# Kernel tuning notes

Hardware: AMD Instinct MI355X
Metric: run time of the kernel (lower is better)

Reference implementation:

```python
import jax, jax.numpy as jnp
import numpy as np

GAMMA = 0.5
LENS = 0.5
WINDOW = 10  # window_size from init

@jax.custom_vjp
def act_fun(x):
    # Heaviside forward, Gaussian surrogate backward (matches torch ActFun)
    return (x > 0).astype(x.dtype)

def _act_fwd(x):
    return act_fun(x), x

def _act_bwd(x, g):
    temp = jnp.exp(-x * x / (2 * LENS * LENS)) / (np.sqrt(2 * np.pi) * LENS)
    return (GAMMA * g * temp,)

act_fun.defvjp(_act_fwd, _act_bwd)

def mem_update(inputs, mem, thr):
    # decay_neu == 1
    mem = mem + inputs
    spike = act_fun(mem - thr)
    mem = mem * (1 - spike)
    neg = (mem < -thr).astype(mem.dtype)
    mem = mem * (1 - neg) - thr * neg
    return mem, spike

def setup_inputs() -> dict:
    key = jax.random.key(0)
    ks = jax.random.split(key, 6)
    B, T, D, H, O = 128, 100, 2048, 1024, 20
    return {
        "input": jax.random.normal(ks[0], (B, T, D), jnp.float32),
        "labels": jax.random.randint(ks[1], (B,), 0, O),
        "hidden_mem": jnp.zeros((B, H), jnp.float32),
        "hidden_spike": jnp.zeros((B, H), jnp.float32),
        "output_mem": jnp.zeros((B, O), jnp.float32),
        "output_spike": jnp.zeros((B, O), jnp.float32),
        "Wi2h": jax.random.normal(ks[2], (H, D), jnp.float32) / np.sqrt(D).astype(np.float32),
        "bi2h": jnp.zeros((H,), jnp.float32),
        "Wh2h": jax.random.normal(ks[3], (H, H), jnp.float32) / np.sqrt(H).astype(np.float32),
        "bh2h": jnp.zeros((H,), jnp.float32),
        "Wh2o": jax.random.normal(ks[4], (O, H), jnp.float32) / np.sqrt(H).astype(np.float32),
        "bh2o": jnp.zeros((O,), jnp.float32),
        "thr_h": jnp.ones((H,), jnp.float32),
        "thr_o": jnp.ones((O,), jnp.float32),
    }

def reference(input, labels, hidden_mem, hidden_spike, output_mem, output_spike,
              Wi2h, bi2h, Wh2h, bh2h, Wh2o, bh2o, thr_h, thr_o):
    B = input.shape[0]

    def step(carry, x_t):
        hm, hs, om, osp, osum = carry
        h_in = x_t @ Wi2h.T + bi2h + hs @ Wh2h.T + bh2h
        hm, hs = mem_update(h_in, hm, thr_h)
        om, osp = mem_update(hs @ Wh2o.T + bh2o, om, thr_o)
        osum = osum + osp
        nbr = (jnp.sum(osp) + jnp.sum(hs)) / B
        return (hm, hs, om, osp, osum), (hs, nbr)

    osum0 = jnp.zeros_like(output_spike)
    carry0 = (hidden_mem, hidden_spike, output_mem, output_spike, osum0)
    (hm, hs, om, osp, osum), (hs_t, nbr_events) = jax.lax.scan(
        step, carry0, jnp.swapaxes(input, 0, 1))  # scan over T

    hidden_spike_t = jnp.transpose(hs_t, (1, 2, 0))  # [B, H, T]
    # moving average over time windows (unfold + mean), stride 1
    c = jnp.cumsum(jnp.pad(hidden_spike_t, ((0, 0), (0, 0), (1, 0))), axis=2)
    hidden_spike_filt = (c[:, :, WINDOW:] - c[:, :, :-WINDOW]) / WINDOW  # [B,H,T-W+1]

    logp = jax.nn.log_softmax(osum, axis=1)
    predictions = jnp.argmax(logp, axis=1)[None, :]  # [1, B]
    loss = -jnp.mean(logp[jnp.arange(B), labels])  # NLLLoss on log_softmax
    return predictions, loss, nbr_events, hidden_spike_filt
```

## Files before the change

kernel.cpp:

```cpp
#include <hip/hip_runtime.h>
#include <hip/hip_bf16.h>
#include <cstdint>
#include <cstddef>

#define B_ 128
#define T_ 100
#define D_ 2048
#define H_ 1024
#define O_ 20
#define H2 512

#define P2NB 256
#define GEMM_NB 800
#define XI_READY 8

typedef float vfloat4 __attribute__((ext_vector_type(4)));

__device__ inline void f4acc(float4& a, const float4 v) {
    a.x += v.x; a.y += v.y; a.z += v.z; a.w += v.w;
}

__global__ __launch_bounds__(256) void prep_kernel(const float* __restrict__ Wh2o,
                                                   float* __restrict__ W2oT,
                                                   float* __restrict__ nbr,
                                                   int* __restrict__ g_flag,
                                                   int* __restrict__ xi_done)
{
    int i = blockIdx.x * 256 + threadIdx.x;
    if (i < H_ * O_) {
        int hh = i / O_;
        int oo = i - hh * O_;
        W2oT[i] = Wh2o[oo * H_ + hh];
    }
    if (i < T_) { nbr[i] = 0.0f; xi_done[i] = 0; }
    if (i < B_ * 2) g_flag[i] = 0;
}

__global__ __launch_bounds__(256) void transpose_kernel(const float* __restrict__ A,
                                                        float* __restrict__ AT)
{
    __shared__ float tile[32][33];
    int bx = blockIdx.x * 32, by = blockIdx.y * 32;
    int tx = threadIdx.x, ty = threadIdx.y;
#pragma unroll
    for (int i = 0; i < 32; i += 8)
        tile[ty + i][tx] = A[(size_t)(by + ty + i) * H_ + bx + tx];
    __syncthreads();
#pragma unroll
    for (int i = 0; i < 32; i += 8)
        AT[(size_t)(bx + ty + i) * H_ + by + tx] = tile[tx][ty + i];
}

__device__ __forceinline__ void gemm_role(int g,
    const float* __restrict__ X, const float* __restrict__ W,
    const float* __restrict__ bi2h, const float* __restrict__ bh2h,
    float* __restrict__ Xi, int* __restrict__ xi_done)
{
    __shared__ float As[16][132];
    __shared__ float Bs[16][132];
    const int t   = g >> 3;
    const int n0  = (g & 7) << 7;
    const int tid = threadIdx.x;
    const int tm8 = (tid >> 5) << 3;
    const int tn4 = (tid & 31) << 2;
    const int ldr = tid >> 2;
    const int ldc = (tid & 3) << 2;

    const float* Xp = X + (size_t)ldr * (T_ * D_) + (size_t)t * D_ + ldc;
    const float* Wp = W + (size_t)(n0 + ldr) * D_ + ldc;

    float acc[8][4];
#pragma unroll
    for (int i = 0; i < 8; ++i)
#pragma unroll
        for (int j = 0; j < 4; ++j) acc[i][j] = 0.0f;

    float4 va = *(const float4*)(Xp);
    float4 vb = *(const float4*)(Wp);
    for (int k0 = 0; k0 < D_; k0 += 16) {
        __syncthreads();
        As[ldc + 0][ldr] = va.x; As[ldc + 1][ldr] = va.y;
        As[ldc + 2][ldr] = va.z; As[ldc + 3][ldr] = va.w;
        Bs[ldc + 0][ldr] = vb.x; Bs[ldc + 1][ldr] = vb.y;
        Bs[ldc + 2][ldr] = vb.z; Bs[ldc + 3][ldr] = vb.w;
        __syncthreads();
        if (k0 + 16 < D_) {
            va = *(const float4*)(Xp + k0 + 16);
            vb = *(const float4*)(Wp + k0 + 16);
        }
#pragma unroll
        for (int k = 0; k < 16; ++k) {
            float4 A0 = *(const float4*)&As[k][tm8];
            float4 A1 = *(const float4*)&As[k][tm8 + 4];
            float4 B0 = *(const float4*)&Bs[k][tn4];
            float a[8] = {A0.x, A0.y, A0.z, A0.w, A1.x, A1.y, A1.z, A1.w};
            float b4[4] = {B0.x, B0.y, B0.z, B0.w};
#pragma unroll
            for (int i = 0; i < 8; ++i)
#pragma unroll
                for (int j = 0; j < 4; ++j) acc[i][j] += a[i] * b4[j];
        }
    }

    float bs[4];
#pragma unroll
    for (int j = 0; j < 4; ++j) {
        int n = n0 + tn4 + j;
        bs[j] = bi2h[n] + bh2h[n];
    }
#pragma unroll
    for (int i = 0; i < 8; ++i) {
        size_t row = (size_t)(tm8 + i) * T_ + t;
        vfloat4 o = {acc[i][0] + bs[0], acc[i][1] + bs[1],
                     acc[i][2] + bs[2], acc[i][3] + bs[3]};
        __builtin_nontemporal_store(o, (vfloat4*)(Xi + row * H_ + n0 + tn4));
    }
    __syncthreads();
    if (tid == 0)
        __hip_atomic_fetch_add(&xi_done[t], 1, __ATOMIC_RELEASE,
                               __HIP_MEMORY_SCOPE_AGENT);
}

__global__ __launch_bounds__(512, 4) void mega_kernel(
    const float* __restrict__ X,
    const float* __restrict__ Wi2h,
    const float* __restrict__ bi2h,
    const float* __restrict__ bh2h,
    float* __restrict__ Xi,
    int* __restrict__ xi_done,
    const float* __restrict__ WT,
    const float* __restrict__ W2oT,
    const float* __restrict__ bh2o,
    const float* __restrict__ thr_h_g,
    const float* __restrict__ thr_o_g,
    const float* __restrict__ hm0,
    const float* __restrict__ hs0,
    const float* __restrict__ om0,
    unsigned long long* __restrict__ g_mask,
    int* __restrict__ g_flag,
    ulonglong2* __restrict__ spk,
    float* __restrict__ osum_out,
    float* __restrict__ nbr_acc)
{
    if (blockIdx.x >= P2NB) {
        gemm_role(blockIdx.x - P2NB, X, Wi2h, bi2h, bh2h, Xi, xi_done);
        return;
    }

    const int pair = blockIdx.x >> 1;
    const int half = blockIdx.x & 1;
    const int b = pair;
    const int tid = threadIdx.x;
    const int lane = tid & 63;
    const int wv = tid >> 6;
    const int h0 = half * H2;
    const int ph0 = h0 ^ H2;
    const int h = h0 + tid;

    __shared__ int   s_list[1024];
    __shared__ float4 s_red[4][128];
    __shared__ unsigned long long s_mask[16];
    __shared__ float s_opart[8][O_];
    __shared__ float s_om[O_], s_osum[O_], s_tho[O_], s_bo[O_];

    float hm = hm0[(size_t)b * H_ + h];
    const float thr = thr_h_g[h];

    if (half == 0 && tid < O_) {
        s_om[tid]   = om0[b * O_ + tid];
        s_osum[tid] = 0.0f;
        s_tho[tid]  = thr_o_g[tid];
        s_bo[tid]   = bh2o[tid];
    }

    {
        bool own = hs0[(size_t)b * H_ + h] > 0.5f;
        bool par = hs0[(size_t)b * H_ + ph0 + tid] > 0.5f;
        unsigned long long mo = __ballot(own), mp = __ballot(par);
        if (lane == 0) { s_mask[half * 8 + wv] = mo; s_mask[(half ^ 1) * 8 + wv] = mp; }
    }
    __syncthreads();

    int cnt_own;
    {
        const int ow = half * 8;
        int pc[8];
#pragma unroll
        for (int k = 0; k < 8; ++k) pc[k] = __popcll(s_mask[ow + k]);
        int basew = 0, tot = 0;
#pragma unroll
        for (int k = 0; k < 8; ++k) { if (k < wv) basew += pc[k]; tot += pc[k]; }
        cnt_own = tot;
        unsigned long long mw = s_mask[ow + wv];
        if ((mw >> lane) & 1ull)
            s_list[basew + __popcll(mw & ((1ull << lane) - 1ull))] = h;
    }
    if (tid == 0) {
        while (__hip_atomic_load(&xi_done[0], __ATOMIC_ACQUIRE,
                                 __HIP_MEMORY_SCOPE_AGENT) < XI_READY)
            __builtin_amdgcn_s_sleep(1);
    }
    __syncthreads();

    const float4* __restrict__ wt4b = (const float4*)WT + (h0 >> 2);
    const int g = tid >> 7;
    const int cid = tid & 127;
    const int fl_partner = pair * 2 + (half ^ 1);
    const int fl_self    = pair * 2 + half;
    unsigned long long bits0 = 0, bits1 = 0;

    for (int t = 0; t <= T_; ++t) {
        const bool full = (t < T_);
        float xi = 0.0f;
        if (full) xi = Xi[((size_t)b * T_ + t) * H_ + h];

        float4 c0 = {0,0,0,0}, c1 = {0,0,0,0}, c2 = {0,0,0,0}, c3 = {0,0,0,0};
        float4 c4 = {0,0,0,0}, c5 = {0,0,0,0}, c6 = {0,0,0,0}, c7 = {0,0,0,0};

        if (full) {
            const int c = cnt_own;
            int l = g;
            for (; l + 28 < c; l += 32) {
                int j0 = s_list[l],      j1 = s_list[l + 4];
                int j2 = s_list[l + 8],  j3 = s_list[l + 12];
                int j4 = s_list[l + 16], j5 = s_list[l + 20];
                int j6 = s_list[l + 24], j7 = s_list[l + 28];
                f4acc(c0, wt4b[(size_t)j0 * 256 + cid]);
                f4acc(c1, wt4b[(size_t)j1 * 256 + cid]);
                f4acc(c2, wt4b[(size_t)j2 * 256 + cid]);
                f4acc(c3, wt4b[(size_t)j3 * 256 + cid]);
                f4acc(c4, wt4b[(size_t)j4 * 256 + cid]);
                f4acc(c5, wt4b[(size_t)j5 * 256 + cid]);
                f4acc(c6, wt4b[(size_t)j6 * 256 + cid]);
                f4acc(c7, wt4b[(size_t)j7 * 256 + cid]);
            }
            for (; l < c; l += 4) f4acc(c0, wt4b[(size_t)s_list[l] * 256 + cid]);
        }

        if (tid == 0) {
            if (t > 0) {
                while (__hip_atomic_load(&g_flag[fl_partner], __ATOMIC_ACQUIRE,
                                         __HIP_MEMORY_SCOPE_AGENT) < t)
                    __builtin_amdgcn_s_sleep(1);
            }
            if (t + 1 < T_) {
                while (__hip_atomic_load(&xi_done[t + 1], __ATOMIC_ACQUIRE,
                                         __HIP_MEMORY_SCOPE_AGENT) < XI_READY)
                    __builtin_amdgcn_s_sleep(1);
            }
        }
        __syncthreads();
        if (t > 0 && tid < 8) {
            const unsigned long long* pm =
                g_mask + (((size_t)(pair * 2 + ((t - 1) & 1)) * 2 + (half ^ 1)) * 8);
            s_mask[(half ^ 1) * 8 + tid] =
                __hip_atomic_load(&pm[tid], __ATOMIC_RELAXED, __HIP_MEMORY_SCOPE_AGENT);
        }
        __syncthreads();

        int cnt_p;
        {
            const int pw = (half ^ 1) * 8;
            int pc[8];
#pragma unroll
            for (int k = 0; k < 8; ++k) pc[k] = __popcll(s_mask[pw + k]);
            int basew = 0, tot = 0;
#pragma unroll
            for (int k = 0; k < 8; ++k) { if (k < wv) basew += pc[k]; tot += pc[k]; }
            cnt_p = tot;
            unsigned long long mw = s_mask[pw + wv];
            if ((mw >> lane) & 1ull)
                s_list[512 + basew + __popcll(mw & ((1ull << lane) - 1ull))] =
                    ph0 + wv * 64 + lane;
        }
        __syncthreads();

        if (full) {
            const int c = cnt_p;
            int l = g;
            for (; l + 28 < c; l += 32) {
                int j0 = s_list[512 + l],      j1 = s_list[512 + l + 4];
                int j2 = s_list[512 + l + 8],  j3 = s_list[512 + l + 12];
                int j4 = s_list[512 + l + 16], j5 = s_list[512 + l + 20];
                int j6 = s_list[512 + l + 24], j7 = s_list[512 + l + 28];
                f4acc(c0, wt4b[(size_t)j0 * 256 + cid]);
                f4acc(c1, wt4b[(size_t)j1 * 256 + cid]);
                f4acc(c2, wt4b[(size_t)j2 * 256 + cid]);
                f4acc(c3, wt4b[(size_t)j3 * 256 + cid]);
                f4acc(c4, wt4b[(size_t)j4 * 256 + cid]);
                f4acc(c5, wt4b[(size_t)j5 * 256 + cid]);
                f4acc(c6, wt4b[(size_t)j6 * 256 + cid]);
                f4acc(c7, wt4b[(size_t)j7 * 256 + cid]);
            }
            for (; l < c; l += 4) f4acc(c0, wt4b[(size_t)s_list[512 + l] * 256 + cid]);
        }

        if (half == 0 && t > 0 && lane < O_) {
            float op = 0.0f;
            for (int q = wv; q < cnt_own; q += 8) op += W2oT[s_list[q] * O_ + lane];
            for (int q = wv; q < cnt_p; q += 8)  op += W2oT[s_list[512 + q] * O_ + lane];
            s_opart[wv][lane] = op;
        }

        {
            f4acc(c0, c1); f4acc(c2, c3); f4acc(c4, c5); f4acc(c6, c7);
            f4acc(c0, c2); f4acc(c4, c6); f4acc(c0, c4);
            s_red[g][cid] = c0;
        }
        const int hidprev = cnt_own + cnt_p;
        __syncthreads();

        if (full) {
            const float* rf = (const float*)s_red;
            float val = rf[tid] + rf[512 + tid] + rf[1024 + tid] + rf[1536 + tid];
            hm += xi + val;
            bool sp = (hm - thr) > 0.0f;
            if (sp) hm = 0.0f;
            if (hm < -thr) hm = -thr;
            if (sp) { if (t < 64) bits0 |= 1ull << t; else bits1 |= 1ull << (t - 64); }
            unsigned long long m = __ballot(sp);
            if (lane == 0) {
                s_mask[half * 8 + wv] = m;
                unsigned long long* gm =
                    g_mask + (((size_t)(pair * 2 + (t & 1)) * 2 + half) * 8);
                __hip_atomic_store(&gm[wv], m, __ATOMIC_RELAXED,
                                   __HIP_MEMORY_SCOPE_AGENT);
            }
        }

        if (half == 0 && t > 0) {
            float osp_l = 0.0f;
            if (tid < O_) {
                float oin = s_bo[tid];
#pragma unroll
                for (int w = 0; w < 8; ++w) oin += s_opart[w][tid];
                float om = s_om[tid] + oin;
                float osp = ((om - s_tho[tid]) > 0.0f) ? 1.0f : 0.0f;
                if (osp > 0.5f) om = 0.0f;
                if (om < -s_tho[tid]) om = -s_tho[tid];
                s_om[tid] = om;
                s_osum[tid] += osp;
                osp_l = osp;
            }
            if (wv == 0) {
                float cc = osp_l;
                cc += __shfl_xor(cc, 1);  cc += __shfl_xor(cc, 2);
                cc += __shfl_xor(cc, 4);  cc += __shfl_xor(cc, 8);
                cc += __shfl_xor(cc, 16); cc += __shfl_xor(cc, 32);
                if (lane == 0)
                    atomicAdd(&nbr_acc[t - 1], cc + (float)hidprev);
            }
        }
        __syncthreads();
        if (full && tid == 0)
            __hip_atomic_store(&g_flag[fl_self], t + 1, __ATOMIC_RELEASE,
                               __HIP_MEMORY_SCOPE_AGENT);
        if (full) {
            const int ow = half * 8;
            int pc[8];
#pragma unroll
            for (int k = 0; k < 8; ++k) pc[k] = __popcll(s_mask[ow + k]);
            int basew = 0, tot = 0;
#pragma unroll
            for (int k = 0; k < 8; ++k) { if (k < wv) basew += pc[k]; tot += pc[k]; }
            cnt_own = tot;
            unsigned long long mw = s_mask[ow + wv];
            if ((mw >> lane) & 1ull)
                s_list[basew + __popcll(mw & ((1ull << lane) - 1ull))] = h;
        }
        __syncthreads();
    }

    ulonglong2 vv; vv.x = bits0; vv.y = bits1;
    spk[(size_t)b * H_ + h] = vv;
    if (half == 0 && tid < O_) osum_out[b * O_ + tid] = s_osum[tid];
}

__global__ __launch_bounds__(256) void filt_kernel(const ulonglong2* __restrict__ spk,
                                                   float* __restrict__ outf)
{
    int i = blockIdx.x * 256 + threadIdx.x;
    ulonglong2 v = spk[i];
    float* o = outf + (size_t)i * 91;
    int s = __popcll(v.x & 0x3FFull);
    o[0] = (float)s * 0.1f;
#pragma unroll 1
    for (int tau = 1; tau <= 90; ++tau) {
        int ta = tau + 9, tsb = tau - 1;
        int add = (ta < 64) ? (int)((v.x >> ta) & 1ull) : (int)((v.y >> (ta - 64)) & 1ull);
        int sub = (tsb < 64) ? (int)((v.x >> tsb) & 1ull) : (int)((v.y >> (tsb - 64)) & 1ull);
        s += add - sub;
        o[tau] = (float)s * 0.1f;
    }
}

__global__ __launch_bounds__(256) void final_kernel(const float* __restrict__ osum,
                                                    const int* __restrict__ labels,
                                                    float* __restrict__ dout)
{
    __shared__ float s_loss[B_];
    int tid = threadIdx.x;
    if (tid < B_) {
        int b = tid;
        float v[O_];
#pragma unroll
        for (int o = 0; o < O_; ++o) v[o] = osum[b * O_ + o];
        float mv = v[0];
        int am = 0;
#pragma unroll
        for (int o = 1; o < O_; ++o)
            if (v[o] > mv) { mv = v[o]; am = o; }
        float se = 0.0f;
#pragma unroll
        for (int o = 0; o < O_; ++o) se += expf(v[o] - mv);
        float lse = mv + logf(se);
        dout[b] = (float)am;
        s_loss[b] = v[labels[b]] - lse;
    }
    if (tid >= 128 && tid < 128 + T_) {
        dout[129 + (tid - 128)] *= (1.0f / (float)B_);
    }
    __syncthreads();
    if (tid == 0) {
        float s = 0.0f;
        for (int b = 0; b < B_; ++b) s += s_loss[b];
        dout[128] = -s / (float)B_;
    }
}

extern "C" void kernel_launch(void* const* d_in, const int* in_sizes, int n_in,
                              void* d_out, int out_size, void* d_ws, size_t ws_size,
                              hipStream_t stream)
{
    const float* input  = (const float*)d_in[0];
    const int*   labels = (const int*)d_in[1];
    const float* hm0    = (const float*)d_in[2];
    const float* hs0    = (const float*)d_in[3];
    const float* om0    = (const float*)d_in[4];
    const float* Wi2h   = (const float*)d_in[6];
    const float* bi2h   = (const float*)d_in[7];
    const float* Wh2h   = (const float*)d_in[8];
    const float* bh2h   = (const float*)d_in[9];
    const float* Wh2o   = (const float*)d_in[10];
    const float* bh2o   = (const float*)d_in[11];
    const float* thr_h  = (const float*)d_in[12];
    const float* thr_o  = (const float*)d_in[13];

    float* out  = (float*)d_out;
    float* nbr  = out + 129;
    float* filt = out + 229;

    char* ws = (char*)d_ws;
    float*      Xi     = (float*)(ws);
    float*      WT     = (float*)(ws + 52428800);
    float*      W2oT   = (float*)(ws + 56623104);
    ulonglong2* spk    = (ulonglong2*)(ws + 56705024);
    float*      osum   = (float*)(ws + 58802176);
    unsigned long long* g_mask = (unsigned long long*)(ws + 58812416);
    int*        g_flag  = (int*)(ws + 58845184);
    int*        xi_done = (int*)(ws + 58846208);

    prep_kernel<<<80, 256, 0, stream>>>(Wh2o, W2oT, nbr, g_flag, xi_done);
    transpose_kernel<<<dim3(32, 32), dim3(32, 8), 0, stream>>>(Wh2h, WT);
    mega_kernel<<<P2NB + GEMM_NB, 512, 0, stream>>>(
        input, Wi2h, bi2h, bh2h, Xi, xi_done,
        WT, W2oT, bh2o, thr_h, thr_o, hm0, hs0, om0,
        g_mask, g_flag, spk, osum, nbr);
    filt_kernel<<<512, 256, 0, stream>>>(spk, filt);
    final_kernel<<<1, 256, 0, stream>>>(osum, labels, out);
}
```

Measured before the change: 2.175 ms.

## Interleave recurrent and GEMM blocks in grid and double-buffer GEMM shared tiles

Block IDs are reassigned so that each group of eight blocks holds four recurrent-role blocks and four input-GEMM blocks. Before, all 256 recurrent blocks came first and the 800 GEMM blocks after them, so the two roles are now spread across CUs and can be co-resident. The grid grows to 1600 blocks, and the surplus blocks exit immediately. The GEMM role also double-buffers its shared-memory tiles, which removes one barrier per k-step at the cost of doubled LDS use.

After: 3.092 ms. 42.1% more time.

```diff
diff --git a/kernel.cpp b/kernel.cpp
--- a/kernel.cpp
+++ b/kernel.cpp
@@ -10,9 +10,9 @@
 #define O_ 20
 #define H2 512
 
-#define P2NB 256
 #define GEMM_NB 800
 #define XI_READY 8
+#define GRID_NB 1600
 
 typedef float vfloat4 __attribute__((ext_vector_type(4)));
 
@@ -56,8 +56,8 @@
     const float* __restrict__ bi2h, const float* __restrict__ bh2h,
     float* __restrict__ Xi, int* __restrict__ xi_done)
 {
-    __shared__ float As[16][132];
-    __shared__ float Bs[16][132];
+    __shared__ float As[2][16][132];
+    __shared__ float Bs[2][16][132];
     const int t   = g >> 3;
     const int n0  = (g & 7) << 7;
     const int tid = threadIdx.x;
@@ -77,22 +77,23 @@
 
     float4 va = *(const float4*)(Xp);
     float4 vb = *(const float4*)(Wp);
-    for (int k0 = 0; k0 < D_; k0 += 16) {
-        __syncthreads();
-        As[ldc + 0][ldr] = va.x; As[ldc + 1][ldr] = va.y;
-        As[ldc + 2][ldr] = va.z; As[ldc + 3][ldr] = va.w;
-        Bs[ldc + 0][ldr] = vb.x; Bs[ldc + 1][ldr] = vb.y;
-        Bs[ldc + 2][ldr] = vb.z; Bs[ldc + 3][ldr] = vb.w;
-        __syncthreads();
-        if (k0 + 16 < D_) {
-            va = *(const float4*)(Xp + k0 + 16);
-            vb = *(const float4*)(Wp + k0 + 16);
-        }
+    constexpr int NT = D_ / 16;
+    for (int tile = 0; tile < NT; ++tile) {
+        const int cur = tile & 1;
+        As[cur][ldc + 0][ldr] = va.x; As[cur][ldc + 1][ldr] = va.y;
+        As[cur][ldc + 2][ldr] = va.z; As[cur][ldc + 3][ldr] = va.w;
+        Bs[cur][ldc + 0][ldr] = vb.x; Bs[cur][ldc + 1][ldr] = vb.y;
+        Bs[cur][ldc + 2][ldr] = vb.z; Bs[cur][ldc + 3][ldr] = vb.w;
+        if (tile + 1 < NT) {
+            va = *(const float4*)(Xp + (tile + 1) * 16);
+            vb = *(const float4*)(Wp + (tile + 1) * 16);
+        }
+        __syncthreads();
 #pragma unroll
         for (int k = 0; k < 16; ++k) {
-            float4 A0 = *(const float4*)&As[k][tm8];
-            float4 A1 = *(const float4*)&As[k][tm8 + 4];
-            float4 B0 = *(const float4*)&Bs[k][tn4];
+            float4 A0 = *(const float4*)&As[cur][k][tm8];
+            float4 A1 = *(const float4*)&As[cur][k][tm8 + 4];
+            float4 B0 = *(const float4*)&Bs[cur][k][tn4];
             float a[8] = {A0.x, A0.y, A0.z, A0.w, A1.x, A1.y, A1.z, A1.w};
             float b4[4] = {B0.x, B0.y, B0.z, B0.w};
 #pragma unroll
@@ -142,13 +143,18 @@
     float* __restrict__ osum_out,
     float* __restrict__ nbr_acc)
 {
-    if (blockIdx.x >= P2NB) {
-        gemm_role(blockIdx.x - P2NB, X, Wi2h, bi2h, bh2h, Xi, xi_done);
+    const int slot = blockIdx.x & 7;
+    const int widx = blockIdx.x >> 3;
+    if (slot >= 4) {
+        int g = widx * 4 + (slot - 4);
+        if (g < GEMM_NB)
+            gemm_role(g, X, Wi2h, bi2h, bh2h, Xi, xi_done);
         return;
     }
-
-    const int pair = blockIdx.x >> 1;
-    const int half = blockIdx.x & 1;
+    if (widx >= 64) return;
+
+    const int pair = widx * 2 + (slot >> 1);
+    const int half = slot & 1;
     const int b = pair;
     const int tid = threadIdx.x;
     const int lane = tid & 63;
@@ -462,7 +468,7 @@
 
     prep_kernel<<<80, 256, 0, stream>>>(Wh2o, W2oT, nbr, g_flag, xi_done);
     transpose_kernel<<<dim3(32, 32), dim3(32, 8), 0, stream>>>(Wh2h, WT);
-    mega_kernel<<<P2NB + GEMM_NB, 512, 0, stream>>>(
+    mega_kernel<<<GRID_NB, 512, 0, stream>>>(
         input, Wi2h, bi2h, bh2h, Xi, xi_done,
         WT, W2oT, bh2o, thr_h, thr_o, hm0, hs0, om0,
         g_mask, g_flag, spk, osum, nbr);
```
